# Optimization experiments

Hardware: AMD Instinct MI355X
Metric: run time of the kernel (lower is better)

## Reference

```python
import jax, jax.numpy as jnp
import numpy as np

N_NODES = 4096
N_EDGES = 262144
D = 128
N_REL = 1000
N_ENT = 50000


def setup_inputs() -> dict:
    key = jax.random.key(0)
    ks = jax.random.split(key, 6)
    x = jax.random.normal(ks[0], (N_NODES, D), dtype=jnp.float32)
    edge_index = jax.random.randint(ks[1], (2, N_EDGES), 0, N_NODES)
    relation_id = jax.random.randint(ks[2], (N_EDGES,), 0, N_REL)
    neg_flag = jax.random.randint(ks[3], (N_EDGES,), 0, 2)
    rel_emb = jax.random.normal(ks[4], (N_REL, D), dtype=jnp.float32)
    entity_emb = jax.random.normal(ks[5], (N_ENT, D), dtype=jnp.float32)
    scale = jnp.ones((N_ENT,), dtype=jnp.float32)
    bias = jnp.zeros((N_ENT,), dtype=jnp.float32)
    return {"x": x, "edge_index": edge_index, "relation_id": relation_id,
            "neg_flag": neg_flag, "rel_emb": rel_emb, "entity_emb": entity_emb,
            "scale": scale, "bias": bias}


def reference(x, edge_index, relation_id, neg_flag, rel_emb, entity_emb, scale, bias):
    src, dst = edge_index[0], edge_index[1]
    # message: gather x_j, TransE tail estimate, sign flip for negated atoms
    neg_coef = 1.0 - 2.0 * neg_flag.astype(x.dtype)           # [E]
    msg = (x[src] + rel_emb[relation_id]) * neg_coef[:, None]  # [E, D]
    # aggregate: scatter-add into target nodes
    aggr_out = jax.ops.segment_sum(msg, dst, num_segments=x.shape[0])  # [N, D]
    # update: residual + bias/scale double-matmul through entity table
    aggr = 0.1 * x + aggr_out                                  # [N, D]
    entity_score = aggr @ entity_emb.T                          # [N, V]
    entity_score = jax.nn.relu(entity_score * scale + bias)
    out = entity_score @ entity_emb                             # [N, D]
    return out
```

## Files before the change

kernel.cpp:

```cpp
#include <hip/hip_runtime.h>
#include <stdint.h>

typedef __attribute__((ext_vector_type(8))) short short8;
typedef __attribute__((ext_vector_type(8))) unsigned short ushort8;
typedef __attribute__((ext_vector_type(4))) float f32x4;

#define NNODES 4096
#define NEDGES 262144
#define DIM 128
#define NENT 50000
#define NENTP 50048
#define NTILES 782
#define NSPLIT 16
#define CHUNK 49

__device__ __forceinline__ unsigned short f2bf(float f) {
  union { __bf16 b; unsigned short u; } c;
  c.b = (__bf16)f;
  return c.u;
}

__global__ __launch_bounds__(256) void k_hist(
    const int* __restrict__ ei, int* __restrict__ cnt)
{
  int e = blockIdx.x * 256 + threadIdx.x;
  atomicAdd(&cnt[ei[NEDGES + e]], 1);
}

__global__ __launch_bounds__(1024) void k_scan(
    const int* __restrict__ cnt, int* __restrict__ off, int* __restrict__ cur)
{
  __shared__ int s[1024];
  int t = threadIdx.x;
  int4 v = reinterpret_cast<const int4*>(cnt)[t];
  int lsum = v.x + v.y + v.z + v.w;
  s[t] = lsum; __syncthreads();
  for (int d = 1; d < 1024; d <<= 1) {
    int a = (t >= d) ? s[t - d] : 0;
    __syncthreads();
    s[t] += a;
    __syncthreads();
  }
  int base = s[t] - lsum;
  int4 o; o.x = base; o.y = base + v.x; o.z = o.y + v.y; o.w = o.z + v.z;
  reinterpret_cast<int4*>(off)[t] = o;
  reinterpret_cast<int4*>(cur)[t] = o;
  if (t == 1023) off[4096] = base + lsum;
}

__global__ __launch_bounds__(256) void k_place(
    const int* __restrict__ ei, const int* __restrict__ rid,
    const int* __restrict__ nf, int* __restrict__ cur, int* __restrict__ sorted)
{
  int e = blockIdx.x * 256 + threadIdx.x;
  int dst = ei[NEDGES + e];
  int pos = atomicAdd(&cur[dst], 1);
  sorted[pos] = ei[e] | (rid[e] << 12) | (nf[e] << 22);
}

__global__ __launch_bounds__(256) void k_aggr(
    const int* __restrict__ off, const int* __restrict__ sorted,
    const float* __restrict__ x, const float* __restrict__ rel,
    unsigned short* __restrict__ q)
{
  __shared__ float sAcc[8 * 132];
  const int n = blockIdx.x;
  const int t = threadIdx.x;
  const int slot = t >> 5;
  const int c = t & 31;
  const int b = off[n], eN = off[n + 1];
  float4 acc = make_float4(0.f, 0.f, 0.f, 0.f);
  for (int i = b + slot; i < eN; i += 8) {
    int p = sorted[i];
    float4 xv = reinterpret_cast<const float4*>(x)[(p & 4095) * 32 + c];
    float4 rv = reinterpret_cast<const float4*>(rel)[((p >> 12) & 1023) * 32 + c];
    float sgn = (p & (1 << 22)) ? -1.f : 1.f;
    acc.x += sgn * (xv.x + rv.x);
    acc.y += sgn * (xv.y + rv.y);
    acc.z += sgn * (xv.z + rv.z);
    acc.w += sgn * (xv.w + rv.w);
  }
  *reinterpret_cast<float4*>(&sAcc[slot * 132 + c * 4]) = acc;
  __syncthreads();
  if (t < 128) {
    float s = 0.f;
#pragma unroll
    for (int k = 0; k < 8; ++k) s += sAcc[k * 132 + t];
    q[n * DIM + t] = f2bf(0.1f * x[n * DIM + t] + s);
  }
}

__global__ __launch_bounds__(256) void k_prep(
    const float* __restrict__ ent, const float* __restrict__ scale,
    unsigned short* __restrict__ ebf, unsigned short* __restrict__ etbf)
{
  __shared__ float sT[64 * 133];
  const int t = threadIdx.x;
  const int e0 = blockIdx.x * 64;
#pragma unroll
  for (int i = 0; i < 8; ++i) {
    int idx = i * 256 + t;
    int e = idx >> 5;
    int c4 = idx & 31;
    float4 v = make_float4(0.f, 0.f, 0.f, 0.f);
    float sc = 0.f;
    if (e0 + e < NENT) {
      v = reinterpret_cast<const float4*>(ent)[(e0 + e) * 32 + c4];
      sc = scale[e0 + e];
    }
    *reinterpret_cast<float4*>(&sT[e * 133 + c4 * 4]) = v;
    ushort4 bq;
    bq.x = f2bf(v.x * sc); bq.y = f2bf(v.y * sc);
    bq.z = f2bf(v.z * sc); bq.w = f2bf(v.w * sc);
    *reinterpret_cast<ushort4*>(&ebf[(e0 + e) * 128 + c4 * 4]) = bq;
  }
  __syncthreads();
  const int lane = t & 63;
  const int w = t >> 6;
  const int dl = lane >> 3;
  const int el = (lane & 7) * 8;
#pragma unroll
  for (int it = 0; it < 4; ++it) {
    int d = it * 32 + w * 8 + dl;
    ushort8 buf;
#pragma unroll
    for (int j = 0; j < 8; ++j) buf[j] = f2bf(sT[(el + j) * 133 + d]);
    *reinterpret_cast<ushort8*>(&etbf[d * NENTP + e0 + el]) = buf;
  }
}

__global__ __launch_bounds__(512, 4) void k_flash(
    const unsigned short* __restrict__ qg,
    const unsigned short* __restrict__ ebf,
    const unsigned short* __restrict__ etbf,
    const float* __restrict__ bias,
    float* __restrict__ out)
{
  __shared__ __align__(16) unsigned short sE[64 * 136];
  __shared__ __align__(16) unsigned short sET[128 * 72];
  __shared__ __align__(16) unsigned short sP[128 * 72];
  __shared__ float sBias[64];

  const int t = threadIdx.x;
  const int lane = t & 63;
  const int w = t >> 6;
  const int wm = w >> 1;
  const int wn = w & 1;
  const int l15 = lane & 15;
  const int quad = lane >> 4;

  const int m0 = blockIdx.x * 128;
  const int tile_lo = blockIdx.y * CHUNK;
  const int tile_hi = (tile_lo + CHUNK < NTILES) ? (tile_lo + CHUNK) : NTILES;

  const int vA0 = t >> 4,          chA0 = t & 15;
  const int vA1 = (512 + t) >> 4,  chA1 = t & 15;
  const int dT0 = t >> 3,          chT0 = t & 7;
  const int dT1 = (512 + t) >> 3,  chT1 = t & 7;

  short8 qf[2][4];
  for (int h = 0; h < 2; ++h) {
#pragma unroll
    for (int i = 0; i < 2; ++i) {
      int idx = i * 512 + t;
      int v = idx >> 4, ch = idx & 15;
      uint4 val = reinterpret_cast<const uint4*>(qg)[(m0 + h * 64 + v) * 16 + ch];
      *reinterpret_cast<uint4*>(&sET[v * 136 + ch * 8]) = val;
    }
    __syncthreads();
    if ((wm >> 1) == h) {
      int lr = (wm & 1) * 32;
#pragma unroll
      for (int tm = 0; tm < 2; ++tm)
#pragma unroll
        for (int kk = 0; kk < 4; ++kk)
          qf[tm][kk] = *reinterpret_cast<const short8*>(
              &sET[(lr + tm * 16 + l15) * 136 + kk * 32 + quad * 8]);
    }
    __syncthreads();
  }

  f32x4 accO[2][4];
#pragma unroll
  for (int tm = 0; tm < 2; ++tm)
#pragma unroll
    for (int td = 0; td < 4; ++td) accO[tm][td] = {0.f, 0.f, 0.f, 0.f};

  uint4 rE0, rE1, rT0, rT1;
  float rB;
  {
    const int vt0 = tile_lo * 64;
    rE0 = *reinterpret_cast<const uint4*>(&ebf[(vt0 + vA0) * 128 + chA0 * 8]);
    rE1 = *reinterpret_cast<const uint4*>(&ebf[(vt0 + vA1) * 128 + chA1 * 8]);
    rT0 = *reinterpret_cast<const uint4*>(&etbf[dT0 * NENTP + vt0 + chT0 * 8]);
    rT1 = *reinterpret_cast<const uint4*>(&etbf[dT1 * NENTP + vt0 + chT1 * 8]);
    rB = (t < 64 && vt0 + t < NENT) ? bias[vt0 + t] : 0.f;
  }

  for (int tile = tile_lo; tile < tile_hi; ++tile) {
    *reinterpret_cast<uint4*>(&sE[vA0 * 136 + chA0 * 8]) = rE0;
    *reinterpret_cast<uint4*>(&sE[vA1 * 136 + chA1 * 8]) = rE1;
    *reinterpret_cast<uint4*>(&sET[dT0 * 72 + chT0 * 8]) = rT0;
    *reinterpret_cast<uint4*>(&sET[dT1 * 72 + chT1 * 8]) = rT1;
    if (t < 64) sBias[t] = rB;
    __syncthreads();

    if (tile + 1 < tile_hi) {
      const int vt0n = (tile + 1) * 64;
      rE0 = *reinterpret_cast<const uint4*>(&ebf[(vt0n + vA0) * 128 + chA0 * 8]);
      rE1 = *reinterpret_cast<const uint4*>(&ebf[(vt0n + vA1) * 128 + chA1 * 8]);
      rT0 = *reinterpret_cast<const uint4*>(&etbf[dT0 * NENTP + vt0n + chT0 * 8]);
      rT1 = *reinterpret_cast<const uint4*>(&etbf[dT1 * NENTP + vt0n + chT1 * 8]);
      rB = (t < 64 && vt0n + t < NENT) ? bias[vt0n + t] : 0.f;
    }

    f32x4 accS[2][2];
#pragma unroll
    for (int tm = 0; tm < 2; ++tm)
#pragma unroll
      for (int tn = 0; tn < 2; ++tn) accS[tm][tn] = {0.f, 0.f, 0.f, 0.f};
#pragma unroll
    for (int kk = 0; kk < 4; ++kk) {
      short8 bE[2];
#pragma unroll
      for (int tn = 0; tn < 2; ++tn)
        bE[tn] = *reinterpret_cast<const short8*>(
            &sE[(wn * 32 + tn * 16 + l15) * 136 + kk * 32 + quad * 8]);
#pragma unroll
      for (int tm = 0; tm < 2; ++tm)
#pragma unroll
        for (int tn = 0; tn < 2; ++tn)
          accS[tm][tn] = __builtin_amdgcn_mfma_f32_16x16x32_bf16(
              qf[tm][kk], bE[tn], accS[tm][tn], 0, 0, 0);
    }

#pragma unroll
    for (int tm = 0; tm < 2; ++tm)
#pragma unroll
      for (int tn = 0; tn < 2; ++tn) {
        int col = wn * 32 + tn * 16 + l15;
        float bs = sBias[col];
#pragma unroll
        for (int r = 0; r < 4; ++r) {
          int row = wm * 32 + tm * 16 + quad * 4 + r;
          sP[row * 72 + col] = f2bf(fmaxf(accS[tm][tn][r] + bs, 0.f));
        }
      }
    __syncthreads();

#pragma unroll
    for (int kk = 0; kk < 2; ++kk) {
      short8 aP[2], bT[4];
#pragma unroll
      for (int tm = 0; tm < 2; ++tm)
        aP[tm] = *reinterpret_cast<const short8*>(
            &sP[(wm * 32 + tm * 16 + l15) * 72 + kk * 32 + quad * 8]);
#pragma unroll
      for (int td = 0; td < 4; ++td)
        bT[td] = *reinterpret_cast<const short8*>(
            &sET[(wn * 64 + td * 16 + l15) * 72 + kk * 32 + quad * 8]);
#pragma unroll
      for (int tm = 0; tm < 2; ++tm)
#pragma unroll
        for (int td = 0; td < 4; ++td)
          accO[tm][td] = __builtin_amdgcn_mfma_f32_16x16x32_bf16(
              aP[tm], bT[td], accO[tm][td], 0, 0, 0);
    }
    __syncthreads();
  }

#pragma unroll
  for (int tm = 0; tm < 2; ++tm)
#pragma unroll
    for (int td = 0; td < 4; ++td)
#pragma unroll
      for (int r = 0; r < 4; ++r) {
        int row = m0 + wm * 32 + tm * 16 + quad * 4 + r;
        int col = wn * 64 + td * 16 + l15;
        atomicAdd(&out[row * DIM + col], accO[tm][td][r]);
      }
}

extern "C" void kernel_launch(void* const* d_in, const int* in_sizes, int n_in,
                              void* d_out, int out_size, void* d_ws, size_t ws_size,
                              hipStream_t stream) {
  const float* x     = (const float*)d_in[0];
  const int*   ei    = (const int*)d_in[1];
  const int*   rid   = (const int*)d_in[2];
  const int*   nf    = (const int*)d_in[3];
  const float* rel   = (const float*)d_in[4];
  const float* ent   = (const float*)d_in[5];
  const float* scale = (const float*)d_in[6];
  const float* bias  = (const float*)d_in[7];
  float* out = (float*)d_out;

  char* ws = (char*)d_ws;
  int*            cnt    = (int*)(ws + 0);
  int*            off    = (int*)(ws + (16u << 10));
  int*            cur    = (int*)(ws + (36u << 10));
  int*            sorted = (int*)(ws + (64u << 10));
  unsigned short* qb     = (unsigned short*)(ws + (1344u << 10));
  unsigned short* ebf    = (unsigned short*)(ws + (2560u << 10));
  unsigned short* etbf   = (unsigned short*)(ws + (2560u << 10) + (size_t)NENTP * DIM * 2);

  hipMemsetAsync(cnt, 0, 4096 * sizeof(int), stream);
  hipMemsetAsync(d_out, 0, (size_t)out_size * sizeof(float), stream);
  k_prep<<<NTILES, 256, 0, stream>>>(ent, scale, ebf, etbf);
  k_hist<<<NEDGES / 256, 256, 0, stream>>>(ei, cnt);
  k_scan<<<1, 1024, 0, stream>>>(cnt, off, cur);
  k_place<<<NEDGES / 256, 256, 0, stream>>>(ei, rid, nf, cur, sorted);
  k_aggr<<<NNODES, 256, 0, stream>>>(off, sorted, x, rel, qb);
  k_flash<<<dim3(NNODES / 128, NSPLIT), 512, 0, stream>>>(qb, ebf, etbf, bias, out);
}
```

Baseline: 282.7 us.

## Fuse histogram into prep, raise split count and occupancy, shrink LDS strides

Merges the edge histogram into the entity prep kernel to remove a launch, raises the vocabulary split from 16 to 24 chunks with a higher waves-per-EU hint, and swaps grid axes so adjacent blocks share entity tiles for L2 reuse. LDS row strides shrink to cut shared memory so more blocks fit per CU. The new strides break 16-byte alignment of the vector LDS accesses, which may force split accesses, and more splits add more atomic output traffic.

After: 634.3 us. 2.24x slower.

```diff
diff --git a/kernel.cpp b/kernel.cpp
--- a/kernel.cpp
+++ b/kernel.cpp
@@ -11,8 +11,11 @@
 #define NENT 50000
 #define NENTP 50048
 #define NTILES 782
-#define NSPLIT 16
-#define CHUNK 49
+#define NSPLIT 24
+#define CHUNK 33
+
+#define SE_S 132
+#define ST_S 68
 
 __device__ __forceinline__ unsigned short f2bf(float f) {
   union { __bf16 b; unsigned short u; } c;
@@ -20,11 +23,50 @@
   return c.u;
 }
 
-__global__ __launch_bounds__(256) void k_hist(
+__global__ __launch_bounds__(256) void k_prep(
+    const float* __restrict__ ent, const float* __restrict__ scale,
+    unsigned short* __restrict__ ebf, unsigned short* __restrict__ etbf,
     const int* __restrict__ ei, int* __restrict__ cnt)
 {
-  int e = blockIdx.x * 256 + threadIdx.x;
-  atomicAdd(&cnt[ei[NEDGES + e]], 1);
+  const int t = threadIdx.x;
+  {
+    int e = blockIdx.x * 256 + t;
+    atomicAdd(&cnt[ei[NEDGES + e]], 1);
+  }
+  if (blockIdx.x >= NTILES) return;
+
+  __shared__ float sT[64 * 133];
+  const int e0 = blockIdx.x * 64;
+#pragma unroll
+  for (int i = 0; i < 8; ++i) {
+    int idx = i * 256 + t;
+    int e = idx >> 5;
+    int c4 = idx & 31;
+    float4 v = make_float4(0.f, 0.f, 0.f, 0.f);
+    float sc = 0.f;
+    if (e0 + e < NENT) {
+      v = reinterpret_cast<const float4*>(ent)[(e0 + e) * 32 + c4];
+      sc = scale[e0 + e];
+    }
+    *reinterpret_cast<float4*>(&sT[e * 133 + c4 * 4]) = v;
+    ushort4 bq;
+    bq.x = f2bf(v.x * sc); bq.y = f2bf(v.y * sc);
+    bq.z = f2bf(v.z * sc); bq.w = f2bf(v.w * sc);
+    *reinterpret_cast<ushort4*>(&ebf[(e0 + e) * 128 + c4 * 4]) = bq;
+  }
+  __syncthreads();
+  const int lane = t & 63;
+  const int w = t >> 6;
+  const int dl = lane >> 3;
+  const int el = (lane & 7) * 8;
+#pragma unroll
+  for (int it = 0; it < 4; ++it) {
+    int d = it * 32 + w * 8 + dl;
+    ushort8 buf;
+#pragma unroll
+    for (int j = 0; j < 8; ++j) buf[j] = f2bf(sT[(el + j) * 133 + d]);
+    *reinterpret_cast<ushort8*>(&etbf[d * NENTP + e0 + el]) = buf;
+  }
 }
 
 __global__ __launch_bounds__(1024) void k_scan(
@@ -90,55 +132,16 @@
   }
 }
 
-__global__ __launch_bounds__(256) void k_prep(
-    const float* __restrict__ ent, const float* __restrict__ scale,
-    unsigned short* __restrict__ ebf, unsigned short* __restrict__ etbf)
-{
-  __shared__ float sT[64 * 133];
-  const int t = threadIdx.x;
-  const int e0 = blockIdx.x * 64;
-#pragma unroll
-  for (int i = 0; i < 8; ++i) {
-    int idx = i * 256 + t;
-    int e = idx >> 5;
-    int c4 = idx & 31;
-    float4 v = make_float4(0.f, 0.f, 0.f, 0.f);
-    float sc = 0.f;
-    if (e0 + e < NENT) {
-      v = reinterpret_cast<const float4*>(ent)[(e0 + e) * 32 + c4];
-      sc = scale[e0 + e];
-    }
-    *reinterpret_cast<float4*>(&sT[e * 133 + c4 * 4]) = v;
-    ushort4 bq;
-    bq.x = f2bf(v.x * sc); bq.y = f2bf(v.y * sc);
-    bq.z = f2bf(v.z * sc); bq.w = f2bf(v.w * sc);
-    *reinterpret_cast<ushort4*>(&ebf[(e0 + e) * 128 + c4 * 4]) = bq;
-  }
-  __syncthreads();
-  const int lane = t & 63;
-  const int w = t >> 6;
-  const int dl = lane >> 3;
-  const int el = (lane & 7) * 8;
-#pragma unroll
-  for (int it = 0; it < 4; ++it) {
-    int d = it * 32 + w * 8 + dl;
-    ushort8 buf;
-#pragma unroll
-    for (int j = 0; j < 8; ++j) buf[j] = f2bf(sT[(el + j) * 133 + d]);
-    *reinterpret_cast<ushort8*>(&etbf[d * NENTP + e0 + el]) = buf;
-  }
-}
-
-__global__ __launch_bounds__(512, 4) void k_flash(
+__global__ __launch_bounds__(512, 6) void k_flash(
     const unsigned short* __restrict__ qg,
     const unsigned short* __restrict__ ebf,
     const unsigned short* __restrict__ etbf,
     const float* __restrict__ bias,
     float* __restrict__ out)
 {
-  __shared__ __align__(16) unsigned short sE[64 * 136];
-  __shared__ __align__(16) unsigned short sET[128 * 72];
-  __shared__ __align__(16) unsigned short sP[128 * 72];
+  __shared__ __align__(16) unsigned short sE[64 * SE_S];
+  __shared__ __align__(16) unsigned short sET[128 * ST_S];
+  __shared__ __align__(16) unsigned short sP[128 * ST_S];
   __shared__ float sBias[64];
 
   const int t = threadIdx.x;
@@ -149,8 +152,8 @@
   const int l15 = lane & 15;
   const int quad = lane >> 4;
 
-  const int m0 = blockIdx.x * 128;
-  const int tile_lo = blockIdx.y * CHUNK;
+  const int m0 = blockIdx.y * 128;
+  const int tile_lo = blockIdx.x * CHUNK;
   const int tile_hi = (tile_lo + CHUNK < NTILES) ? (tile_lo + CHUNK) : NTILES;
 
   const int vA0 = t >> 4,          chA0 = t & 15;
@@ -165,7 +168,7 @@
       int idx = i * 512 + t;
       int v = idx >> 4, ch = idx & 15;
       uint4 val = reinterpret_cast<const uint4*>(qg)[(m0 + h * 64 + v) * 16 + ch];
-      *reinterpret_cast<uint4*>(&sET[v * 136 + ch * 8]) = val;
+      *reinterpret_cast<uint4*>(&sE[v * SE_S + ch * 8]) = val;
     }
     __syncthreads();
     if ((wm >> 1) == h) {
@@ -175,7 +178,7 @@
 #pragma unroll
         for (int kk = 0; kk < 4; ++kk)
           qf[tm][kk] = *reinterpret_cast<const short8*>(
-              &sET[(lr + tm * 16 + l15) * 136 + kk * 32 + quad * 8]);
+              &sE[(lr + tm * 16 + l15) * SE_S + kk * 32 + quad * 8]);
     }
     __syncthreads();
   }
@@ -198,10 +201,10 @@
   }
 
   for (int tile = tile_lo; tile < tile_hi; ++tile) {
-    *reinterpret_cast<uint4*>(&sE[vA0 * 136 + chA0 * 8]) = rE0;
-    *reinterpret_cast<uint4*>(&sE[vA1 * 136 + chA1 * 8]) = rE1;
-    *reinterpret_cast<uint4*>(&sET[dT0 * 72 + chT0 * 8]) = rT0;
-    *reinterpret_cast<uint4*>(&sET[dT1 * 72 + chT1 * 8]) = rT1;
+    *reinterpret_cast<uint4*>(&sE[vA0 * SE_S + chA0 * 8]) = rE0;
+    *reinterpret_cast<uint4*>(&sE[vA1 * SE_S + chA1 * 8]) = rE1;
+    *reinterpret_cast<uint4*>(&sET[dT0 * ST_S + chT0 * 8]) = rT0;
+    *reinterpret_cast<uint4*>(&sET[dT1 * ST_S + chT1 * 8]) = rT1;
     if (t < 64) sBias[t] = rB;
     __syncthreads();
 
@@ -225,7 +228,7 @@
 #pragma unroll
       for (int tn = 0; tn < 2; ++tn)
         bE[tn] = *reinterpret_cast<const short8*>(
-            &sE[(wn * 32 + tn * 16 + l15) * 136 + kk * 32 + quad * 8]);
+            &sE[(wn * 32 + tn * 16 + l15) * SE_S + kk * 32 + quad * 8]);
 #pragma unroll
       for (int tm = 0; tm < 2; ++tm)
 #pragma unroll
@@ -243,7 +246,7 @@
 #pragma unroll
         for (int r = 0; r < 4; ++r) {
           int row = wm * 32 + tm * 16 + quad * 4 + r;
-          sP[row * 72 + col] = f2bf(fmaxf(accS[tm][tn][r] + bs, 0.f));
+          sP[row * ST_S + col] = f2bf(fmaxf(accS[tm][tn][r] + bs, 0.f));
         }
       }
     __syncthreads();
@@ -254,11 +257,11 @@
 #pragma unroll
       for (int tm = 0; tm < 2; ++tm)
         aP[tm] = *reinterpret_cast<const short8*>(
-            &sP[(wm * 32 + tm * 16 + l15) * 72 + kk * 32 + quad * 8]);
+            &sP[(wm * 32 + tm * 16 + l15) * ST_S + kk * 32 + quad * 8]);
 #pragma unroll
       for (int td = 0; td < 4; ++td)
         bT[td] = *reinterpret_cast<const short8*>(
-            &sET[(wn * 64 + td * 16 + l15) * 72 + kk * 32 + quad * 8]);
+            &sET[(wn * 64 + td * 16 + l15) * ST_S + kk * 32 + quad * 8]);
 #pragma unroll
       for (int tm = 0; tm < 2; ++tm)
 #pragma unroll
@@ -305,10 +308,9 @@
 
   hipMemsetAsync(cnt, 0, 4096 * sizeof(int), stream);
   hipMemsetAsync(d_out, 0, (size_t)out_size * sizeof(float), stream);
-  k_prep<<<NTILES, 256, 0, stream>>>(ent, scale, ebf, etbf);
-  k_hist<<<NEDGES / 256, 256, 0, stream>>>(ei, cnt);
+  k_prep<<<NEDGES / 256, 256, 0, stream>>>(ent, scale, ebf, etbf, ei, cnt);
   k_scan<<<1, 1024, 0, stream>>>(cnt, off, cur);
   k_place<<<NEDGES / 256, 256, 0, stream>>>(ei, rid, nf, cur, sorted);
   k_aggr<<<NNODES, 256, 0, stream>>>(off, sorted, x, rel, qb);
-  k_flash<<<dim3(NNODES / 128, NSPLIT), 512, 0, stream>>>(qb, ebf, etbf, bias, out);
-}
+  k_flash<<<dim3(NSPLIT, NNODES / 128), 512, 0, stream>>>(qb, ebf, etbf, bias, out);
+}
```
